# Optimization experiments

Hardware: AMD Instinct MI355X
Metric: run time of the kernel (lower is better)

## Reference

```python
import jax, jax.numpy as jnp
import numpy as np

B, N, C, K = 8, 4096, 512, 150

def setup_inputs() -> dict:
    key = jax.random.key(0)
    ks = jax.random.split(key, 10)
    std_c = float(np.sqrt(2.0 / C))
    x = jax.random.normal(ks[0], (B, N, C), dtype=jnp.float32)
    Wq = jax.random.normal(ks[1], (K, C), dtype=jnp.float32) * std_c
    bq = jnp.zeros((K,), dtype=jnp.float32)
    Wk = jax.random.normal(ks[2], (K, C), dtype=jnp.float32) * std_c
    bk = jnp.zeros((K,), dtype=jnp.float32)
    Wv = jax.random.normal(ks[3], (C, C), dtype=jnp.float32) * std_c
    bv = jnp.zeros((C,), dtype=jnp.float32)
    # original inits mlp_res to zeros; use small random so output is nontrivial
    Wres = jax.random.normal(ks[4], (C, C), dtype=jnp.float32) * (0.02)
    bres = jnp.zeros((C,), dtype=jnp.float32)
    gamma = jnp.full((1,), 0.5, dtype=jnp.float32)  # original init is 0; nonzero for testing
    return {"x": x, "Wq": Wq, "bq": bq, "Wk": Wk, "bk": bk,
            "Wv": Wv, "bv": bv, "Wres": Wres, "bres": bres, "gamma": gamma}

def reference(x, Wq, bq, Wk, bk, Wv, bv, Wres, bres, gamma):
    # seg_map: (B,N,K); seg_ft: (B,N,K); feats: (B,N,C)
    seg_map = jnp.einsum('bnc,kc->bnk', x, Wq) + bq
    seg_ft = jnp.einsum('bnc,kc->bnk', x, Wk) + bk
    v = jnp.einsum('bnc,dc->bnd', x, Wv) + bv
    # low-rank QK^T -> (B,N,N), unscaled, row softmax
    score = jnp.einsum('bnk,bmk->bnm', seg_map, seg_ft)
    score = jax.nn.softmax(score, axis=-1)
    feats = jnp.einsum('bnm,bmd->bnd', score, v)
    feats = jnp.einsum('bnd,ed->bne', feats, Wres) + bres
    # dropout omitted (inference); gamma-gated residual
    feat_map = gamma * feats + x
    return (seg_map, feat_map)
```

## Files before the change

kernel.cpp:

```cpp
#include <hip/hip_runtime.h>
#include <cstdint>
#include <cstddef>

#define M_ROWS 32768
#define CDIM   512
#define KRANK  150
#define KPAD   160

typedef __bf16 bf16x8 __attribute__((ext_vector_type(8)));
typedef float  f32x4  __attribute__((ext_vector_type(4)));

union U16B { uint4 u; bf16x8 b; };
static __device__ __forceinline__ bf16x8 u2b(uint4 u) { U16B x; x.u = u; return x.b; }

static __device__ __forceinline__ unsigned short f2bf(float f) {
  uint32_t u = __float_as_uint(f);
  u += 0x7fffu + ((u >> 16) & 1u);
  return (unsigned short)(u >> 16);
}

static __device__ __forceinline__ void cvt8(float4 a, float4 b, uint4& h, uint4& l) {
  float v[8] = {a.x, a.y, a.z, a.w, b.x, b.y, b.z, b.w};
  unsigned short hs[8], ls[8];
#pragma unroll
  for (int i = 0; i < 8; ++i) {
    hs[i] = f2bf(v[i]);
    const float hf = __uint_as_float((uint32_t)hs[i] << 16);
    ls[i] = f2bf(v[i] - hf);
  }
  h = *(uint4*)&hs[0];
  l = *(uint4*)&ls[0];
}

static __device__ __forceinline__ void glds16(const void* g, void* l) {
  __builtin_amdgcn_global_load_lds(
      (const __attribute__((address_space(1))) unsigned int*)g,
      (__attribute__((address_space(3))) unsigned int*)l, 16, 0, 0);
}

static __device__ __forceinline__ int sa16f(int row, int k4) {
  return ((row >> 1) << 3) + ((((row & 1) << 2) | k4) ^ ((row >> 1) & 7));
}

__global__ __launch_bounds__(512)
void cvt_w(const float* __restrict__ Wv, const float* __restrict__ Wres,
           const float* __restrict__ Wq, const float* __restrict__ Wk,
           unsigned short* __restrict__ WvC, unsigned short* __restrict__ WresC,
           unsigned short* __restrict__ WqC, unsigned short* __restrict__ WkC)
{
  int job = blockIdx.x;
  const float* W; unsigned short* img; int N;
  if (job < 32)      { W = Wv;   img = WvC;   N = 512; }
  else if (job < 64) { W = Wres; img = WresC; N = 512; job -= 32; }
  else if (job < 80) { W = Wq;   img = WqC;   N = KRANK; job -= 64; }
  else               { W = Wk;   img = WkC;   N = KRANK; job -= 80; }
  const int nt = (N == 512) ? (job >> 4) : 0;
  const int kt = job & 15;

  const int tid = threadIdx.x;
  const int srow = tid >> 2, sk4 = tid & 3;
  const int sa = sa16f(srow, sk4);
  unsigned short* ib = img + (size_t)(nt * 16 + kt) * 16384;
#pragma unroll
  for (int h = 0; h < 2; ++h) {
    const int row = nt * 256 + h * 128 + srow;
    float4 v0 = make_float4(0.f, 0.f, 0.f, 0.f), v1 = v0;
    if (row < N) {
      v0 = *(const float4*)&W[(size_t)row * 512 + kt * 32 + sk4 * 8];
      v1 = *(const float4*)&W[(size_t)row * 512 + kt * 32 + sk4 * 8 + 4];
    }
    uint4 h4, l4; cvt8(v0, v1, h4, l4);
    const int cell = h * 512 + sa;
    *(uint4*)&ib[(size_t)cell * 8]          = h4;
    *(uint4*)&ib[(size_t)(1024 + cell) * 8] = l4;
  }
}

template<int MODE>
__global__ __launch_bounds__(512, 4)
void mgemm_nt(const float* __restrict__ A, const unsigned short* __restrict__ Wimg,
              const float* __restrict__ bias, float* __restrict__ out,
              const float* __restrict__ xres, const float* __restrict__ gammap,
              unsigned short* __restrict__ aux)
{
  __shared__ __align__(16) unsigned short lds[24576];
  const int tid = threadIdx.x;
  const int m0  = blockIdx.y * 128;

  const int srow = tid >> 2, sk4 = tid & 3;
  const int sa16 = sa16f(srow, sk4);
  const float* ap = A + (size_t)(m0 + srow) * 512 + sk4 * 8;

  const int lane = tid & 63, w = tid >> 6;
  const int wm = w >> 2, wn = w & 3;
  const int cq = lane & 15, quad = lane >> 4;
  const int fsub = (((cq & 1) << 2) | quad) ^ (cq >> 1);
  const int a16 = wm * 256 + ((cq >> 1) << 3) + fsub;
  const int b16 = wn * 256 + ((cq >> 1) << 3) + fsub;

  const unsigned short* ibase = Wimg + (size_t)(blockIdx.x * 16) * 16384
                              + (size_t)(w * 64 + lane) * 8;

  f32x4 acc[4][4];
#pragma unroll
  for (int i = 0; i < 4; ++i)
#pragma unroll
    for (int j = 0; j < 4; ++j) acc[i][j] = (f32x4){0.f, 0.f, 0.f, 0.f};

  for (int kt = 0; kt < 512; kt += 32) {
    const float4 av0 = *(const float4*)(ap + kt);
    const float4 av1 = *(const float4*)(ap + kt + 4);
    uint4 ahi, alo;
    cvt8(av0, av1, ahi, alo);

    __syncthreads();
    *(uint4*)&lds[       sa16 * 8] = ahi;
    *(uint4*)&lds[4096 + sa16 * 8] = alo;
    const unsigned short* src = ibase + (size_t)(kt >> 5) * 16384;
#pragma unroll
    for (int c = 0; c < 4; ++c)
      glds16(src + (size_t)c * 4096, &lds[8192 + (c * 512 + w * 64) * 8]);
    __syncthreads();

    bf16x8 ah[4], al_[4];
#pragma unroll
    for (int i = 0; i < 4; ++i) {
      ah[i]  = u2b(*(const uint4*)&lds[       (a16 + i * 64) * 8]);
      al_[i] = u2b(*(const uint4*)&lds[4096 + (a16 + i * 64) * 8]);
    }
#pragma unroll
    for (int j = 0; j < 4; ++j) {
      const bf16x8 bh = u2b(*(const uint4*)&lds[8192  + (b16 + j * 64) * 8]);
      const bf16x8 bl = u2b(*(const uint4*)&lds[16384 + (b16 + j * 64) * 8]);
#pragma unroll
      for (int i = 0; i < 4; ++i) {
        acc[i][j] = __builtin_amdgcn_mfma_f32_16x16x32_bf16(ah[i],  bh, acc[i][j], 0, 0, 0);
        acc[i][j] = __builtin_amdgcn_mfma_f32_16x16x32_bf16(al_[i], bh, acc[i][j], 0, 0, 0);
        acc[i][j] = __builtin_amdgcn_mfma_f32_16x16x32_bf16(ah[i],  bl, acc[i][j], 0, 0, 0);
      }
    }
  }

  const int n0b = blockIdx.x * 256;
  const int mb = m0 + wm * 64 + quad * 4;
  const int nb = n0b + wn * 64 + cq;

  if (MODE == 1) {
    const float g = gammap[0];
#pragma unroll
    for (int j = 0; j < 4; ++j) {
      const float bvj = bias[nb + j * 16];
#pragma unroll
      for (int i = 0; i < 4; ++i) {
#pragma unroll
        for (int r = 0; r < 4; ++r) {
          const size_t off = (size_t)(mb + i * 16 + r) * 512 + (nb + j * 16);
          out[off] = fmaf(g, acc[i][j][r] + bvj, xres[off]);
        }
      }
    }
  } else if (MODE == 4) {
    const int b = m0 >> 12;
    const int key0 = (m0 & 4095) + wm * 64 + quad * 4;
#pragma unroll
    for (int j = 0; j < 4; ++j) {
      const float bvj = bias[nb + j * 16];
      const size_t rowo = (size_t)(b * 512 + nb + j * 16) * 4096;
#pragma unroll
      for (int i = 0; i < 4; ++i) {
        unsigned short o4[4];
#pragma unroll
        for (int r = 0; r < 4; ++r) o4[r] = f2bf(acc[i][j][r] + bvj);
        uint2 o;
        o.x = (unsigned int)o4[0] | ((unsigned int)o4[1] << 16);
        o.y = (unsigned int)o4[2] | ((unsigned int)o4[3] << 16);
        *(uint2*)&aux[rowo + key0 + i * 16] = o;
      }
    }
  } else {
#pragma unroll
    for (int j = 0; j < 4; ++j) {
      const int n = nb + j * 16;
      if (n < KPAD) {
        const float bvj = (n < KRANK) ? bias[n] : 0.f;
#pragma unroll
        for (int i = 0; i < 4; ++i) {
#pragma unroll
          for (int r = 0; r < 4; ++r) {
            const int m = mb + i * 16 + r;
            float v = (n < KRANK) ? (acc[i][j][r] + bvj) : 0.f;
            if (MODE == 2 && n < KRANK) out[(size_t)m * KRANK + n] = v;
            const unsigned short h = f2bf(v);
            aux[(size_t)m * 320 + n] = h;
            const float hf = __uint_as_float(((uint32_t)h) << 16);
            aux[(size_t)m * 320 + 160 + n] = f2bf(v - hf);
          }
        }
      }
    }
  }
}

__global__ __launch_bounds__(512, 2)
void attn_mfma(const unsigned short* __restrict__ Qc,
               const unsigned short* __restrict__ Kc,
               const unsigned short* __restrict__ VT,
               float* __restrict__ O)
{
  __shared__ __align__(16) unsigned short smem[32592];
  unsigned short* klds = smem;
  unsigned short* vtl  = smem + 10496;
  unsigned short* plds = smem + 26944;
  float*    alw   = (float*)(smem + 32064);
  unsigned* updf  = (unsigned*)(smem + 32320);
  float*    linvp = (float*)(smem + 32336);

  const int bid = blockIdx.x;
  const int b   = bid & 7;
  const int qt  = bid >> 3;
  const int r0  = (b << 12) + qt * 128;

  const int tid  = threadIdx.x;
  const int w    = tid >> 6;
  const int lane = tid & 63;
  const int quad = lane >> 4;
  const int cq   = lane & 15;
  const int p    = w >> 1;
  const int h    = w & 1;

  bf16x8 qhi[5], qlo[5];
  {
    const size_t qrow = (size_t)(r0 + w * 16 + cq) * 320;
#pragma unroll
    for (int c = 0; c < 5; ++c) {
      qhi[c] = u2b(*(const uint4*)(Qc + qrow + c * 32 + quad * 8));
      qlo[c] = u2b(*(const uint4*)(Qc + qrow + 160 + c * 32 + quad * 8));
    }
  }

  f32x4 acc4[32];
#pragma unroll
  for (int i = 0; i < 32; ++i) acc4[i] = (f32x4){0.f, 0.f, 0.f, 0.f};
  float mreg[4], lreg[4];
#pragma unroll
  for (int r = 0; r < 4; ++r) { mreg[r] = -3.0e38f; lreg[r] = 0.f; }

  const int vqd = (tid & 3) * 8;
  const int vc  = tid >> 2;
  const int vwb = (tid & 3) * 4112 + vc * 8;
  const int vrb = quad * 4112 + h * 2048 + cq * 8;

  const int krow0 = tid / 40,          kc0 = (tid - krow0 * 40) * 8;
  const int krow1 = (tid + 512) / 40,  kc1 = ((tid + 512) - krow1 * 40) * 8;
  const int krow2 = (tid + 1024) / 40, kc2 = ((tid + 1024) - krow2 * 40) * 8;

  uint4 os; os.x = os.y = os.z = os.w = 0x3F803F80u;
  const bf16x8 vone = u2b(os);

  uint4 pk0, pk1, pk2, pv0, pv1, pv2, pv3;
  const unsigned short* kbase = Kc + (size_t)(b * 4096) * 320;
  const unsigned short* vbase = VT + ((size_t)(b * 512 + vc)) * 4096 + vqd;
  {
    pk0 = *(const uint4*)(kbase + (size_t)tid * 8);
    pk1 = *(const uint4*)(kbase + (size_t)(tid + 512) * 8);
    if (tid < 256) pk2 = *(const uint4*)(kbase + (size_t)(tid + 1024) * 8);
    pv0 = *(const uint4*)(vbase);
    pv1 = *(const uint4*)(vbase + (size_t)128 * 4096);
    pv2 = *(const uint4*)(vbase + (size_t)256 * 4096);
    pv3 = *(const uint4*)(vbase + (size_t)384 * 4096);
  }

  for (int kt = 0; kt < 128; ++kt) {
    __syncthreads();

    *(uint4*)&klds[krow0 * 328 + kc0] = pk0;
    *(uint4*)&klds[krow1 * 328 + kc1] = pk1;
    if (tid < 256) *(uint4*)&klds[krow2 * 328 + kc2] = pk2;
    *(uint4*)&vtl[vwb]        = pv0;
    *(uint4*)&vtl[vwb + 1024] = pv1;
    *(uint4*)&vtl[vwb + 2048] = pv2;
    *(uint4*)&vtl[vwb + 3072] = pv3;

    __syncthreads();

    {
      const int ktn = (kt < 127) ? kt + 1 : 127;
      pk0 = *(const uint4*)(kbase + (size_t)(ktn * 32 * 320) + (size_t)tid * 8);
      pk1 = *(const uint4*)(kbase + (size_t)(ktn * 32 * 320) + (size_t)(tid + 512) * 8);
      if (tid < 256) pk2 = *(const uint4*)(kbase + (size_t)(ktn * 32 * 320) + (size_t)(tid + 1024) * 8);
      pv0 = *(const uint4*)(vbase + ktn * 32);
      pv1 = *(const uint4*)(vbase + (size_t)128 * 4096 + ktn * 32);
      pv2 = *(const uint4*)(vbase + (size_t)256 * 4096 + ktn * 32);
      pv3 = *(const uint4*)(vbase + (size_t)384 * 4096 + ktn * 32);
    }

    f32x4 S0 = (f32x4){0.f, 0.f, 0.f, 0.f};
    f32x4 S1 = (f32x4){0.f, 0.f, 0.f, 0.f};
    __builtin_amdgcn_s_setprio(1);
#pragma unroll
    for (int c = 0; c < 5; ++c) {
      const int ko = c * 32 + quad * 8;
      const bf16x8 kh0 = u2b(*(const uint4*)&klds[cq * 328 + ko]);
      const bf16x8 kl0 = u2b(*(const uint4*)&klds[cq * 328 + 160 + ko]);
      const bf16x8 kh1 = u2b(*(const uint4*)&klds[(16 + cq) * 328 + ko]);
      const bf16x8 kl1 = u2b(*(const uint4*)&klds[(16 + cq) * 328 + 160 + ko]);
      S0 = __builtin_amdgcn_mfma_f32_16x16x32_bf16(qhi[c], kh0, S0, 0, 0, 0);
      S1 = __builtin_amdgcn_mfma_f32_16x16x32_bf16(qhi[c], kh1, S1, 0, 0, 0);
      S0 = __builtin_amdgcn_mfma_f32_16x16x32_bf16(qhi[c], kl0, S0, 0, 0, 0);
      S1 = __builtin_amdgcn_mfma_f32_16x16x32_bf16(qhi[c], kl1, S1, 0, 0, 0);
      S0 = __builtin_amdgcn_mfma_f32_16x16x32_bf16(qlo[c], kh0, S0, 0, 0, 0);
      S1 = __builtin_amdgcn_mfma_f32_16x16x32_bf16(qlo[c], kh1, S1, 0, 0, 0);
    }
    __builtin_amdgcn_s_setprio(0);

    unsigned short* pw = plds + w * 640;
    float alph[4];
    bool upd = false;
#pragma unroll
    for (int r = 0; r < 4; ++r) {
      const float s0 = S0[r], s1 = S1[r];
      float t = fmaxf(s0, s1);
      t = fmaxf(t, __shfl_xor(t, 1));
      t = fmaxf(t, __shfl_xor(t, 2));
      t = fmaxf(t, __shfl_xor(t, 4));
      t = fmaxf(t, __shfl_xor(t, 8));
      const float mo = mreg[r];
      const bool need = (t > mo + 8.f);
      const float mn = need ? t : mo;
      upd = upd || need;
      alph[r] = need ? __expf(mo - mn) : 1.f;
      mreg[r] = mn;
      const float p0 = __expf(s0 - mn);
      const float p1 = __expf(s1 - mn);
      const int prow = (quad * 4 + r) * 40;
      pw[prow + cq]      = f2bf(p0);
      pw[prow + 16 + cq] = f2bf(p1);
    }

    {
      const bf16x8 pa_self = u2b(*(const uint4*)&pw[cq * 40 + quad * 8]);
      f32x4 sum4 = (f32x4){0.f, 0.f, 0.f, 0.f};
      sum4 = __builtin_amdgcn_mfma_f32_16x16x32_bf16(pa_self, vone, sum4, 0, 0, 0);
#pragma unroll
      for (int r = 0; r < 4; ++r) lreg[r] = lreg[r] * alph[r] + sum4[r];
    }
    if (cq == 0) {
#pragma unroll
      for (int r = 0; r < 4; ++r) alw[w * 16 + quad * 4 + r] = alph[r];
    }
    const bool anyu = __any(upd);
    if (lane == 0) updf[w] = anyu ? 1u : 0u;

    __syncthreads();

    const unsigned short* pb = plds + (2 * p) * 640 + cq * 40 + quad * 8;
    const bf16x8 pa0 = u2b(*(const uint4*)pb);
    const bf16x8 pa1 = u2b(*(const uint4*)(pb + 640));

    if (updf[2 * p] | updf[2 * p + 1]) {
      float aA[4], aB[4];
#pragma unroll
      for (int r = 0; r < 4; ++r) {
        aA[r] = alw[(2 * p) * 16 + quad * 4 + r];
        aB[r] = alw[(2 * p + 1) * 16 + quad * 4 + r];
      }
#pragma unroll
      for (int ct = 0; ct < 16; ++ct) {
#pragma unroll
        for (int r = 0; r < 4; ++r) {
          acc4[ct][r]      *= aA[r];
          acc4[16 + ct][r] *= aB[r];
        }
      }
    }

    __builtin_amdgcn_s_setprio(1);
#pragma unroll
    for (int ct = 0; ct < 16; ++ct) {
      const bf16x8 vb = u2b(*(const uint4*)&vtl[vrb + ct * 128]);
      acc4[ct]      = __builtin_amdgcn_mfma_f32_16x16x32_bf16(pa0, vb, acc4[ct], 0, 0, 0);
      acc4[16 + ct] = __builtin_amdgcn_mfma_f32_16x16x32_bf16(pa1, vb, acc4[16 + ct], 0, 0, 0);
    }
    __builtin_amdgcn_s_setprio(0);
  }

  if (cq == 0) {
#pragma unroll
    for (int r = 0; r < 4; ++r) linvp[w * 16 + quad * 4 + r] = 1.f / lreg[r];
  }
  __syncthreads();

  float invv[2][4];
#pragma unroll
  for (int rt = 0; rt < 2; ++rt)
#pragma unroll
    for (int r = 0; r < 4; ++r)
      invv[rt][r] = linvp[(2 * p + rt) * 16 + quad * 4 + r];

  float* ep = (float*)smem + w * 1088;
#pragma unroll
  for (int rt = 0; rt < 2; ++rt) {
    const int rowb = r0 + (2 * p + rt) * 16;
#pragma unroll
    for (int g = 0; g < 4; ++g) {
#pragma unroll
      for (int ii = 0; ii < 4; ++ii)
#pragma unroll
        for (int r = 0; r < 4; ++r)
          ep[(quad * 4 + r) * 68 + ii * 16 + cq] = acc4[rt * 16 + g * 4 + ii][r] * invv[rt][r];
#pragma unroll
      for (int t = 0; t < 4; ++t) {
        const int flat4 = t * 64 + lane;
        const int row = flat4 >> 4;
        const int c4 = flat4 & 15;
        const float4 val = *(const float4*)&ep[row * 68 + c4 * 4];
        *(float4*)&O[(size_t)(rowb + row) * CDIM + h * 256 + g * 64 + c4 * 4] = val;
      }
    }
  }
}

extern "C" void kernel_launch(void* const* d_in, const int* in_sizes, int n_in,
                              void* d_out, int out_size, void* d_ws, size_t ws_size,
                              hipStream_t stream)
{
  const float* x     = (const float*)d_in[0];
  const float* Wq    = (const float*)d_in[1];
  const float* bq    = (const float*)d_in[2];
  const float* Wk    = (const float*)d_in[3];
  const float* bk    = (const float*)d_in[4];
  const float* Wv    = (const float*)d_in[5];
  const float* bv    = (const float*)d_in[6];
  const float* Wres  = (const float*)d_in[7];
  const float* bres  = (const float*)d_in[8];
  const float* gamma = (const float*)d_in[9];

  float* seg_map  = (float*)d_out;
  float* feat_map = seg_map + (size_t)M_ROWS * KRANK;

  unsigned short* Qcomb = (unsigned short*)d_ws;
  unsigned short* Kcomb = Qcomb + (size_t)M_ROWS * 320;
  unsigned short* VTb   = Kcomb + (size_t)M_ROWS * 320;
  float*          feats = (float*)(VTb + (size_t)M_ROWS * CDIM);
  unsigned short* WvC   = (unsigned short*)(feats + (size_t)M_ROWS * CDIM);
  unsigned short* WresC = WvC   + (size_t)2 * 16 * 16384;
  unsigned short* WqC   = WresC + (size_t)2 * 16 * 16384;
  unsigned short* WkC   = WqC   + (size_t)16 * 16384;

  cvt_w<<<dim3(96), dim3(512), 0, stream>>>(Wv, Wres, Wq, Wk, WvC, WresC, WqC, WkC);
  mgemm_nt<2><<<dim3(1, 256), dim3(512), 0, stream>>>(x, WqC, bq, seg_map, nullptr, nullptr, Qcomb);
  mgemm_nt<3><<<dim3(1, 256), dim3(512), 0, stream>>>(x, WkC, bk, nullptr, nullptr, nullptr, Kcomb);
  mgemm_nt<4><<<dim3(2, 256), dim3(512), 0, stream>>>(x, WvC, bv, nullptr, nullptr, nullptr, VTb);
  attn_mfma<<<dim3(256), dim3(512), 0, stream>>>(Qcomb, Kcomb, VTb, feats);
  mgemm_nt<1><<<dim3(2, 256), dim3(512), 0, stream>>>(feats, WresC, bres, feat_map, x, gamma, nullptr);
}
```

Baseline: 769.2 us.

## Fuse Q/K projections, register-prefetch GEMM tiles, and rebalance attention warp tiling

Q and K projection GEMMs are merged into one launch, with blockIdx.x choosing the weight image, bias and output. The GEMM main loop drops the direct global-to-LDS loads and instead prefetches the next A and B tiles into registers while the current tile is being computed, so global latency overlaps the MFMAs. The attention kernel now gives each wave 4 row tiles by 8 column tiles instead of 2 by 16, which reuses each V fragment across more MFMAs. It also replaces two shuffles with DPP ops and packs the update flags into bytes. In exchange, the prefetch raises register pressure, and the new attention split changes how LDS is read.

```diff
diff --git a/kernel.cpp b/kernel.cpp
--- a/kernel.cpp
+++ b/kernel.cpp
@@ -32,10 +32,10 @@
   l = *(uint4*)&ls[0];
 }
 
-static __device__ __forceinline__ void glds16(const void* g, void* l) {
-  __builtin_amdgcn_global_load_lds(
-      (const __attribute__((address_space(1))) unsigned int*)g,
-      (__attribute__((address_space(3))) unsigned int*)l, 16, 0, 0);
+template<int CTRL>
+static __device__ __forceinline__ float dppx(float x) {
+  return __uint_as_float((unsigned)__builtin_amdgcn_update_dpp(
+      0, (int)__float_as_uint(x), CTRL, 0xf, 0xf, true));
 }
 
 static __device__ __forceinline__ int sa16f(int row, int k4) {
@@ -81,15 +81,26 @@
 void mgemm_nt(const float* __restrict__ A, const unsigned short* __restrict__ Wimg,
               const float* __restrict__ bias, float* __restrict__ out,
               const float* __restrict__ xres, const float* __restrict__ gammap,
-              unsigned short* __restrict__ aux)
+              unsigned short* __restrict__ aux,
+              const unsigned short* __restrict__ Wimg2,
+              const float* __restrict__ bias2,
+              unsigned short* __restrict__ aux2)
 {
   __shared__ __align__(16) unsigned short lds[24576];
   const int tid = threadIdx.x;
   const int m0  = blockIdx.y * 128;
+  const int bx  = blockIdx.x;
+
+  const unsigned short* img = (MODE == 5) ? (bx ? Wimg2 : Wimg)
+                                          : Wimg + (size_t)(bx * 16) * 16384;
+  const float* bias_u = (MODE == 5 && bx) ? bias2 : bias;
+  unsigned short* aux_u = (MODE == 5 && bx) ? aux2 : aux;
 
   const int srow = tid >> 2, sk4 = tid & 3;
   const int sa16 = sa16f(srow, sk4);
   const float* ap = A + (size_t)(m0 + srow) * 512 + sk4 * 8;
+
+  const unsigned short* ibp = img + (size_t)tid * 8;
 
   const int lane = tid & 63, w = tid >> 6;
   const int wm = w >> 2, wn = w & 3;
@@ -98,29 +109,41 @@
   const int a16 = wm * 256 + ((cq >> 1) << 3) + fsub;
   const int b16 = wn * 256 + ((cq >> 1) << 3) + fsub;
 
-  const unsigned short* ibase = Wimg + (size_t)(blockIdx.x * 16) * 16384
-                              + (size_t)(w * 64 + lane) * 8;
-
   f32x4 acc[4][4];
 #pragma unroll
   for (int i = 0; i < 4; ++i)
 #pragma unroll
     for (int j = 0; j < 4; ++j) acc[i][j] = (f32x4){0.f, 0.f, 0.f, 0.f};
 
+  float4 a0 = *(const float4*)(ap);
+  float4 a1 = *(const float4*)(ap + 4);
+  uint4 b0 = *(const uint4*)(ibp);
+  uint4 b1 = *(const uint4*)(ibp + 4096);
+  uint4 b2 = *(const uint4*)(ibp + 8192);
+  uint4 b3 = *(const uint4*)(ibp + 12288);
+
   for (int kt = 0; kt < 512; kt += 32) {
-    const float4 av0 = *(const float4*)(ap + kt);
-    const float4 av1 = *(const float4*)(ap + kt + 4);
     uint4 ahi, alo;
-    cvt8(av0, av1, ahi, alo);
+    cvt8(a0, a1, ahi, alo);
 
     __syncthreads();
     *(uint4*)&lds[       sa16 * 8] = ahi;
     *(uint4*)&lds[4096 + sa16 * 8] = alo;
-    const unsigned short* src = ibase + (size_t)(kt >> 5) * 16384;
-#pragma unroll
-    for (int c = 0; c < 4; ++c)
-      glds16(src + (size_t)c * 4096, &lds[8192 + (c * 512 + w * 64) * 8]);
+    *(uint4*)&lds[8192  + tid * 8]         = b0;
+    *(uint4*)&lds[8192  + tid * 8 + 4096]  = b1;
+    *(uint4*)&lds[8192  + tid * 8 + 8192]  = b2;
+    *(uint4*)&lds[8192  + tid * 8 + 12288] = b3;
     __syncthreads();
+
+    if (kt < 480) {
+      a0 = *(const float4*)(ap + kt + 32);
+      a1 = *(const float4*)(ap + kt + 36);
+      const unsigned short* nip = ibp + (size_t)((kt >> 5) + 1) * 16384;
+      b0 = *(const uint4*)(nip);
+      b1 = *(const uint4*)(nip + 4096);
+      b2 = *(const uint4*)(nip + 8192);
+      b3 = *(const uint4*)(nip + 12288);
+    }
 
     bf16x8 ah[4], al_[4];
 #pragma unroll
@@ -141,7 +164,7 @@
     }
   }
 
-  const int n0b = blockIdx.x * 256;
+  const int n0b = (MODE == 5) ? 0 : bx * 256;
   const int mb = m0 + wm * 64 + quad * 4;
   const int nb = n0b + wn * 64 + cq;
 
@@ -149,7 +172,7 @@
     const float g = gammap[0];
 #pragma unroll
     for (int j = 0; j < 4; ++j) {
-      const float bvj = bias[nb + j * 16];
+      const float bvj = bias_u[nb + j * 16];
 #pragma unroll
       for (int i = 0; i < 4; ++i) {
 #pragma unroll
@@ -164,7 +187,7 @@
     const int key0 = (m0 & 4095) + wm * 64 + quad * 4;
 #pragma unroll
     for (int j = 0; j < 4; ++j) {
-      const float bvj = bias[nb + j * 16];
+      const float bvj = bias_u[nb + j * 16];
       const size_t rowo = (size_t)(b * 512 + nb + j * 16) * 4096;
 #pragma unroll
       for (int i = 0; i < 4; ++i) {
@@ -174,7 +197,7 @@
         uint2 o;
         o.x = (unsigned int)o4[0] | ((unsigned int)o4[1] << 16);
         o.y = (unsigned int)o4[2] | ((unsigned int)o4[3] << 16);
-        *(uint2*)&aux[rowo + key0 + i * 16] = o;
+        *(uint2*)&aux_u[rowo + key0 + i * 16] = o;
       }
     }
   } else {
@@ -182,18 +205,18 @@
     for (int j = 0; j < 4; ++j) {
       const int n = nb + j * 16;
       if (n < KPAD) {
-        const float bvj = (n < KRANK) ? bias[n] : 0.f;
+        const float bvj = (n < KRANK) ? bias_u[n] : 0.f;
 #pragma unroll
         for (int i = 0; i < 4; ++i) {
 #pragma unroll
           for (int r = 0; r < 4; ++r) {
             const int m = mb + i * 16 + r;
             float v = (n < KRANK) ? (acc[i][j][r] + bvj) : 0.f;
-            if (MODE == 2 && n < KRANK) out[(size_t)m * KRANK + n] = v;
+            if (bx == 0 && n < KRANK) out[(size_t)m * KRANK + n] = v;
             const unsigned short h = f2bf(v);
-            aux[(size_t)m * 320 + n] = h;
+            aux_u[(size_t)m * 320 + n] = h;
             const float hf = __uint_as_float(((uint32_t)h) << 16);
-            aux[(size_t)m * 320 + 160 + n] = f2bf(v - hf);
+            aux_u[(size_t)m * 320 + 160 + n] = f2bf(v - hf);
           }
         }
       }
@@ -212,8 +235,8 @@
   unsigned short* vtl  = smem + 10496;
   unsigned short* plds = smem + 26944;
   float*    alw   = (float*)(smem + 32064);
-  unsigned* updf  = (unsigned*)(smem + 32320);
-  float*    linvp = (float*)(smem + 32336);
+  unsigned char* updb = (unsigned char*)(smem + 32320);
+  float*    linvp = (float*)(smem + 32324);
 
   const int bid = blockIdx.x;
   const int b   = bid & 7;
@@ -225,8 +248,8 @@
   const int lane = tid & 63;
   const int quad = lane >> 4;
   const int cq   = lane & 15;
-  const int p    = w >> 1;
-  const int h    = w & 1;
+  const int p    = w >> 2;
+  const int cqt  = w & 3;
 
   bf16x8 qhi[5], qlo[5];
   {
@@ -248,7 +271,7 @@
   const int vqd = (tid & 3) * 8;
   const int vc  = tid >> 2;
   const int vwb = (tid & 3) * 4112 + vc * 8;
-  const int vrb = quad * 4112 + h * 2048 + cq * 8;
+  const int vrb = quad * 4112 + cqt * 1024 + cq * 8;
 
   const int krow0 = tid / 40,          kc0 = (tid - krow0 * 40) * 8;
   const int krow1 = (tid + 512) / 40,  kc1 = ((tid + 512) - krow1 * 40) * 8;
@@ -320,8 +343,8 @@
     for (int r = 0; r < 4; ++r) {
       const float s0 = S0[r], s1 = S1[r];
       float t = fmaxf(s0, s1);
-      t = fmaxf(t, __shfl_xor(t, 1));
-      t = fmaxf(t, __shfl_xor(t, 2));
+      t = fmaxf(t, dppx<0xB1>(t));
+      t = fmaxf(t, dppx<0x4E>(t));
       t = fmaxf(t, __shfl_xor(t, 4));
       t = fmaxf(t, __shfl_xor(t, 8));
       const float mo = mreg[r];
@@ -349,37 +372,39 @@
       for (int r = 0; r < 4; ++r) alw[w * 16 + quad * 4 + r] = alph[r];
     }
     const bool anyu = __any(upd);
-    if (lane == 0) updf[w] = anyu ? 1u : 0u;
+    if (lane == 0) updb[w] = anyu ? 1 : 0;
 
     __syncthreads();
 
-    const unsigned short* pb = plds + (2 * p) * 640 + cq * 40 + quad * 8;
-    const bf16x8 pa0 = u2b(*(const uint4*)pb);
-    const bf16x8 pa1 = u2b(*(const uint4*)(pb + 640));
-
-    if (updf[2 * p] | updf[2 * p + 1]) {
-      float aA[4], aB[4];
-#pragma unroll
-      for (int r = 0; r < 4; ++r) {
-        aA[r] = alw[(2 * p) * 16 + quad * 4 + r];
-        aB[r] = alw[(2 * p + 1) * 16 + quad * 4 + r];
-      }
-#pragma unroll
-      for (int ct = 0; ct < 16; ++ct) {
-#pragma unroll
-        for (int r = 0; r < 4; ++r) {
-          acc4[ct][r]      *= aA[r];
-          acc4[16 + ct][r] *= aB[r];
-        }
-      }
+    const unsigned short* pb = plds + (4 * p) * 640 + cq * 40 + quad * 8;
+    bf16x8 pa[4];
+#pragma unroll
+    for (int rt = 0; rt < 4; ++rt) pa[rt] = u2b(*(const uint4*)(pb + rt * 640));
+
+    const uint2 uu = *(const uint2*)updb;
+    if (p ? uu.y : uu.x) {
+      float aT[4][4];
+#pragma unroll
+      for (int rt = 0; rt < 4; ++rt)
+#pragma unroll
+        for (int r = 0; r < 4; ++r)
+          aT[rt][r] = alw[(4 * p + rt) * 16 + quad * 4 + r];
+#pragma unroll
+      for (int rt = 0; rt < 4; ++rt)
+#pragma unroll
+        for (int ct = 0; ct < 8; ++ct)
+#pragma unroll
+          for (int r = 0; r < 4; ++r)
+            acc4[rt * 8 + ct][r] *= aT[rt][r];
     }
 
     __builtin_amdgcn_s_setprio(1);
 #pragma unroll
-    for (int ct = 0; ct < 16; ++ct) {
+    for (int ct = 0; ct < 8; ++ct) {
       const bf16x8 vb = u2b(*(const uint4*)&vtl[vrb + ct * 128]);
-      acc4[ct]      = __builtin_amdgcn_mfma_f32_16x16x32_bf16(pa0, vb, acc4[ct], 0, 0, 0);
-      acc4[16 + ct] = __builtin_amdgcn_mfma_f32_16x16x32_bf16(pa1, vb, acc4[16 + ct], 0, 0, 0);
+#pragma unroll
+      for (int rt = 0; rt < 4; ++rt)
+        acc4[rt * 8 + ct] = __builtin_amdgcn_mfma_f32_16x16x32_bf16(pa[rt], vb, acc4[rt * 8 + ct], 0, 0, 0);
     }
     __builtin_amdgcn_s_setprio(0);
   }
@@ -390,31 +415,31 @@
   }
   __syncthreads();
 
-  float invv[2][4];
-#pragma unroll
-  for (int rt = 0; rt < 2; ++rt)
+  float invv[4][4];
+#pragma unroll
+  for (int rt = 0; rt < 4; ++rt)
 #pragma unroll
     for (int r = 0; r < 4; ++r)
-      invv[rt][r] = linvp[(2 * p + rt) * 16 + quad * 4 + r];
+      invv[rt][r] = linvp[(4 * p + rt) * 16 + quad * 4 + r];
 
   float* ep = (float*)smem + w * 1088;
 #pragma unroll
-  for (int rt = 0; rt < 2; ++rt) {
-    const int rowb = r0 + (2 * p + rt) * 16;
-#pragma unroll
-    for (int g = 0; g < 4; ++g) {
+  for (int rt = 0; rt < 4; ++rt) {
+    const int rowb = r0 + (4 * p + rt) * 16;
+#pragma unroll
+    for (int g = 0; g < 2; ++g) {
 #pragma unroll
       for (int ii = 0; ii < 4; ++ii)
 #pragma unroll
         for (int r = 0; r < 4; ++r)
-          ep[(quad * 4 + r) * 68 + ii * 16 + cq] = acc4[rt * 16 + g * 4 + ii][r] * invv[rt][r];
+          ep[(quad * 4 + r) * 68 + ii * 16 + cq] = acc4[rt * 8 + g * 4 + ii][r] * invv[rt][r];
 #pragma unroll
       for (int t = 0; t < 4; ++t) {
         const int flat4 = t * 64 + lane;
         const int row = flat4 >> 4;
         const int c4 = flat4 & 15;
         const float4 val = *(const float4*)&ep[row * 68 + c4 * 4];
-        *(float4*)&O[(size_t)(rowb + row) * CDIM + h * 256 + g * 64 + c4 * 4] = val;
+        *(float4*)&O[(size_t)(rowb + row) * CDIM + cqt * 128 + g * 64 + c4 * 4] = val;
       }
     }
   }
@@ -448,9 +473,8 @@
   unsigned short* WkC   = WqC   + (size_t)16 * 16384;
 
   cvt_w<<<dim3(96), dim3(512), 0, stream>>>(Wv, Wres, Wq, Wk, WvC, WresC, WqC, WkC);
-  mgemm_nt<2><<<dim3(1, 256), dim3(512), 0, stream>>>(x, WqC, bq, seg_map, nullptr, nullptr, Qcomb);
-  mgemm_nt<3><<<dim3(1, 256), dim3(512), 0, stream>>>(x, WkC, bk, nullptr, nullptr, nullptr, Kcomb);
-  mgemm_nt<4><<<dim3(2, 256), dim3(512), 0, stream>>>(x, WvC, bv, nullptr, nullptr, nullptr, VTb);
+  mgemm_nt<5><<<dim3(2, 256), dim3(512), 0, stream>>>(x, WqC, bq, seg_map, nullptr, nullptr, Qcomb, WkC, bk, Kcomb);
+  mgemm_nt<4><<<dim3(2, 256), dim3(512), 0, stream>>>(x, WvC, bv, nullptr, nullptr, nullptr, VTb, nullptr, nullptr, nullptr);
   attn_mfma<<<dim3(256), dim3(512), 0, stream>>>(Qcomb, Kcomb, VTb, feats);
-  mgemm_nt<1><<<dim3(2, 256), dim3(512), 0, stream>>>(feats, WresC, bres, feat_map, x, gamma, nullptr);
-}
+  mgemm_nt<1><<<dim3(2, 256), dim3(512), 0, stream>>>(feats, WresC, bres, feat_map, x, gamma, nullptr, nullptr, nullptr, nullptr);
+}
```

Result: slower. 843.5 us (+9.7%).

## Preconvert x to split-bf16 image, merge Q/K GEMMs, split score accumulators, use DPP

Applied to the files above, without the earlier changes.

A new kernel converts x once into a swizzled hi/lo bf16 tile image, stored in the feats workspace. The projection GEMMs then load A tiles straight into LDS with global_load_lds instead of each reconverting fp32 x. The Q and K projections are merged into one launch selected by blockIdx.x. In attention, the three score MFMA chains per tile get separate accumulators to break dependency stalls, and the first two max-reduction shuffles become DPP ops. This trades an extra pass writing and reading the x image for less repeated conversion work and fewer launches.

```diff
diff --git a/kernel.cpp b/kernel.cpp
--- a/kernel.cpp
+++ b/kernel.cpp
@@ -36,6 +36,12 @@
   __builtin_amdgcn_global_load_lds(
       (const __attribute__((address_space(1))) unsigned int*)g,
       (__attribute__((address_space(3))) unsigned int*)l, 16, 0, 0);
+}
+
+template<int CTRL>
+static __device__ __forceinline__ float dppx(float x) {
+  return __uint_as_float((unsigned)__builtin_amdgcn_update_dpp(
+      0, (int)__float_as_uint(x), CTRL, 0xf, 0xf, true));
 }
 
 static __device__ __forceinline__ int sa16f(int row, int k4) {
@@ -76,16 +82,43 @@
   }
 }
 
-template<int MODE>
+__global__ __launch_bounds__(512)
+void cvt_x(const float* __restrict__ X, unsigned short* __restrict__ Ximg)
+{
+  const int bid = blockIdx.x;
+  const int mt = bid >> 4, kt = bid & 15;
+  const int tid = threadIdx.x;
+  const int srow = tid >> 2, sk4 = tid & 3;
+  const int sa = sa16f(srow, sk4);
+  const float* xp = X + (size_t)(mt * 128 + srow) * 512 + kt * 32 + sk4 * 8;
+  const float4 v0 = *(const float4*)(xp);
+  const float4 v1 = *(const float4*)(xp + 4);
+  uint4 h4, l4; cvt8(v0, v1, h4, l4);
+  unsigned short* ib = Ximg + (size_t)bid * 8192;
+  *(uint4*)&ib[(size_t)sa * 8]          = h4;
+  *(uint4*)&ib[(size_t)(512 + sa) * 8]  = l4;
+}
+
+template<int MODE, int AGL>
 __global__ __launch_bounds__(512, 4)
-void mgemm_nt(const float* __restrict__ A, const unsigned short* __restrict__ Wimg,
+void mgemm_nt(const float* __restrict__ A, const unsigned short* __restrict__ Ximg,
+              const unsigned short* __restrict__ Wimg,
               const float* __restrict__ bias, float* __restrict__ out,
               const float* __restrict__ xres, const float* __restrict__ gammap,
-              unsigned short* __restrict__ aux)
+              unsigned short* __restrict__ aux,
+              const unsigned short* __restrict__ Wimg2,
+              const float* __restrict__ bias2,
+              unsigned short* __restrict__ aux2)
 {
   __shared__ __align__(16) unsigned short lds[24576];
   const int tid = threadIdx.x;
   const int m0  = blockIdx.y * 128;
+  const int bx  = blockIdx.x;
+
+  const unsigned short* img = (MODE == 5) ? (bx ? Wimg2 : Wimg)
+                                          : Wimg + (size_t)(bx * 16) * 16384;
+  const float* bias_u = (MODE == 5 && bx) ? bias2 : bias;
+  unsigned short* aux_u = (MODE == 5 && bx) ? aux2 : aux;
 
   const int srow = tid >> 2, sk4 = tid & 3;
   const int sa16 = sa16f(srow, sk4);
@@ -98,8 +131,9 @@
   const int a16 = wm * 256 + ((cq >> 1) << 3) + fsub;
   const int b16 = wn * 256 + ((cq >> 1) << 3) + fsub;
 
-  const unsigned short* ibase = Wimg + (size_t)(blockIdx.x * 16) * 16384
-                              + (size_t)(w * 64 + lane) * 8;
+  const unsigned short* ibase = img + (size_t)(w * 64 + lane) * 8;
+  const unsigned short* xibase = Ximg + (size_t)(m0 >> 7) * 16 * 8192
+                               + (size_t)(w * 64 + lane) * 8;
 
   f32x4 acc[4][4];
 #pragma unroll
@@ -108,14 +142,22 @@
     for (int j = 0; j < 4; ++j) acc[i][j] = (f32x4){0.f, 0.f, 0.f, 0.f};
 
   for (int kt = 0; kt < 512; kt += 32) {
-    const float4 av0 = *(const float4*)(ap + kt);
-    const float4 av1 = *(const float4*)(ap + kt + 4);
     uint4 ahi, alo;
-    cvt8(av0, av1, ahi, alo);
+    if (AGL == 0) {
+      const float4 av0 = *(const float4*)(ap + kt);
+      const float4 av1 = *(const float4*)(ap + kt + 4);
+      cvt8(av0, av1, ahi, alo);
+    }
 
     __syncthreads();
-    *(uint4*)&lds[       sa16 * 8] = ahi;
-    *(uint4*)&lds[4096 + sa16 * 8] = alo;
+    if (AGL == 0) {
+      *(uint4*)&lds[       sa16 * 8] = ahi;
+      *(uint4*)&lds[4096 + sa16 * 8] = alo;
+    } else {
+      const unsigned short* xs = xibase + (size_t)(kt >> 5) * 8192;
+      glds16(xs,                         &lds[(w * 64) * 8]);
+      glds16(xs + (size_t)512 * 8,       &lds[4096 + (w * 64) * 8]);
+    }
     const unsigned short* src = ibase + (size_t)(kt >> 5) * 16384;
 #pragma unroll
     for (int c = 0; c < 4; ++c)
@@ -141,7 +183,7 @@
     }
   }
 
-  const int n0b = blockIdx.x * 256;
+  const int n0b = (MODE == 5) ? 0 : bx * 256;
   const int mb = m0 + wm * 64 + quad * 4;
   const int nb = n0b + wn * 64 + cq;
 
@@ -149,7 +191,7 @@
     const float g = gammap[0];
 #pragma unroll
     for (int j = 0; j < 4; ++j) {
-      const float bvj = bias[nb + j * 16];
+      const float bvj = bias_u[nb + j * 16];
 #pragma unroll
       for (int i = 0; i < 4; ++i) {
 #pragma unroll
@@ -164,7 +206,7 @@
     const int key0 = (m0 & 4095) + wm * 64 + quad * 4;
 #pragma unroll
     for (int j = 0; j < 4; ++j) {
-      const float bvj = bias[nb + j * 16];
+      const float bvj = bias_u[nb + j * 16];
       const size_t rowo = (size_t)(b * 512 + nb + j * 16) * 4096;
 #pragma unroll
       for (int i = 0; i < 4; ++i) {
@@ -174,7 +216,7 @@
         uint2 o;
         o.x = (unsigned int)o4[0] | ((unsigned int)o4[1] << 16);
         o.y = (unsigned int)o4[2] | ((unsigned int)o4[3] << 16);
-        *(uint2*)&aux[rowo + key0 + i * 16] = o;
+        *(uint2*)&aux_u[rowo + key0 + i * 16] = o;
       }
     }
   } else {
@@ -182,18 +224,18 @@
     for (int j = 0; j < 4; ++j) {
       const int n = nb + j * 16;
       if (n < KPAD) {
-        const float bvj = (n < KRANK) ? bias[n] : 0.f;
+        const float bvj = (n < KRANK) ? bias_u[n] : 0.f;
 #pragma unroll
         for (int i = 0; i < 4; ++i) {
 #pragma unroll
           for (int r = 0; r < 4; ++r) {
             const int m = mb + i * 16 + r;
             float v = (n < KRANK) ? (acc[i][j][r] + bvj) : 0.f;
-            if (MODE == 2 && n < KRANK) out[(size_t)m * KRANK + n] = v;
+            if (bx == 0 && n < KRANK) out[(size_t)m * KRANK + n] = v;
             const unsigned short h = f2bf(v);
-            aux[(size_t)m * 320 + n] = h;
+            aux_u[(size_t)m * 320 + n] = h;
             const float hf = __uint_as_float(((uint32_t)h) << 16);
-            aux[(size_t)m * 320 + 160 + n] = f2bf(v - hf);
+            aux_u[(size_t)m * 320 + 160 + n] = f2bf(v - hf);
           }
         }
       }
@@ -294,8 +336,8 @@
       pv3 = *(const uint4*)(vbase + (size_t)384 * 4096 + ktn * 32);
     }
 
-    f32x4 S0 = (f32x4){0.f, 0.f, 0.f, 0.f};
-    f32x4 S1 = (f32x4){0.f, 0.f, 0.f, 0.f};
+    f32x4 cA0 = (f32x4){0.f, 0.f, 0.f, 0.f}, cB0 = cA0, cC0 = cA0;
+    f32x4 cA1 = cA0, cB1 = cA0, cC1 = cA0;
     __builtin_amdgcn_s_setprio(1);
 #pragma unroll
     for (int c = 0; c < 5; ++c) {
@@ -304,14 +346,16 @@
       const bf16x8 kl0 = u2b(*(const uint4*)&klds[cq * 328 + 160 + ko]);
       const bf16x8 kh1 = u2b(*(const uint4*)&klds[(16 + cq) * 328 + ko]);
       const bf16x8 kl1 = u2b(*(const uint4*)&klds[(16 + cq) * 328 + 160 + ko]);
-      S0 = __builtin_amdgcn_mfma_f32_16x16x32_bf16(qhi[c], kh0, S0, 0, 0, 0);
-      S1 = __builtin_amdgcn_mfma_f32_16x16x32_bf16(qhi[c], kh1, S1, 0, 0, 0);
-      S0 = __builtin_amdgcn_mfma_f32_16x16x32_bf16(qhi[c], kl0, S0, 0, 0, 0);
-      S1 = __builtin_amdgcn_mfma_f32_16x16x32_bf16(qhi[c], kl1, S1, 0, 0, 0);
-      S0 = __builtin_amdgcn_mfma_f32_16x16x32_bf16(qlo[c], kh0, S0, 0, 0, 0);
-      S1 = __builtin_amdgcn_mfma_f32_16x16x32_bf16(qlo[c], kh1, S1, 0, 0, 0);
+      cA0 = __builtin_amdgcn_mfma_f32_16x16x32_bf16(qhi[c], kh0, cA0, 0, 0, 0);
+      cA1 = __builtin_amdgcn_mfma_f32_16x16x32_bf16(qhi[c], kh1, cA1, 0, 0, 0);
+      cB0 = __builtin_amdgcn_mfma_f32_16x16x32_bf16(qhi[c], kl0, cB0, 0, 0, 0);
+      cB1 = __builtin_amdgcn_mfma_f32_16x16x32_bf16(qhi[c], kl1, cB1, 0, 0, 0);
+      cC0 = __builtin_amdgcn_mfma_f32_16x16x32_bf16(qlo[c], kh0, cC0, 0, 0, 0);
+      cC1 = __builtin_amdgcn_mfma_f32_16x16x32_bf16(qlo[c], kh1, cC1, 0, 0, 0);
     }
     __builtin_amdgcn_s_setprio(0);
+    const f32x4 S0 = (cA0 + cB0) + cC0;
+    const f32x4 S1 = (cA1 + cB1) + cC1;
 
     unsigned short* pw = plds + w * 640;
     float alph[4];
@@ -320,8 +364,8 @@
     for (int r = 0; r < 4; ++r) {
       const float s0 = S0[r], s1 = S1[r];
       float t = fmaxf(s0, s1);
-      t = fmaxf(t, __shfl_xor(t, 1));
-      t = fmaxf(t, __shfl_xor(t, 2));
+      t = fmaxf(t, dppx<0xB1>(t));
+      t = fmaxf(t, dppx<0x4E>(t));
       t = fmaxf(t, __shfl_xor(t, 4));
       t = fmaxf(t, __shfl_xor(t, 8));
       const float mo = mreg[r];
@@ -446,11 +490,12 @@
   unsigned short* WresC = WvC   + (size_t)2 * 16 * 16384;
   unsigned short* WqC   = WresC + (size_t)2 * 16 * 16384;
   unsigned short* WkC   = WqC   + (size_t)16 * 16384;
+  unsigned short* XiC   = (unsigned short*)feats;
 
   cvt_w<<<dim3(96), dim3(512), 0, stream>>>(Wv, Wres, Wq, Wk, WvC, WresC, WqC, WkC);
-  mgemm_nt<2><<<dim3(1, 256), dim3(512), 0, stream>>>(x, WqC, bq, seg_map, nullptr, nullptr, Qcomb);
-  mgemm_nt<3><<<dim3(1, 256), dim3(512), 0, stream>>>(x, WkC, bk, nullptr, nullptr, nullptr, Kcomb);
-  mgemm_nt<4><<<dim3(2, 256), dim3(512), 0, stream>>>(x, WvC, bv, nullptr, nullptr, nullptr, VTb);
+  cvt_x<<<dim3(4096), dim3(512), 0, stream>>>(x, XiC);
+  mgemm_nt<5, 1><<<dim3(2, 256), dim3(512), 0, stream>>>(x, XiC, WqC, bq, seg_map, nullptr, nullptr, Qcomb, WkC, bk, Kcomb);
+  mgemm_nt<4, 1><<<dim3(2, 256), dim3(512), 0, stream>>>(x, XiC, WvC, bv, nullptr, nullptr, nullptr, VTb, nullptr, nullptr, nullptr);
   attn_mfma<<<dim3(256), dim3(512), 0, stream>>>(Qcomb, Kcomb, VTb, feats);
-  mgemm_nt<1><<<dim3(2, 256), dim3(512), 0, stream>>>(feats, WresC, bres, feat_map, x, gamma, nullptr);
-}
+  mgemm_nt<1, 0><<<dim3(2, 256), dim3(512), 0, stream>>>(feats, nullptr, WresC, bres, feat_map, x, gamma, nullptr, nullptr, nullptr, nullptr);
+}
```

After: 794.8 us. +3.3%, slower.
